# Kernel tuning notes

Hardware: AMD Instinct MI355X
Metric: run time of the kernel (lower is better)

## Reference

```python
import jax, jax.numpy as jnp
import numpy as np

B, H, S, D = 1, 16, 2048, 128
NUM_DOCS = 4


def setup_inputs() -> dict:
    key = jax.random.key(0)
    kq, kk, kv = jax.random.split(key, 3)
    q = jax.random.normal(kq, (B, H, S, D), dtype=jnp.float32)
    k = jax.random.normal(kk, (B, H, S, D), dtype=jnp.float32)
    v = jax.random.normal(kv, (B, H, S, D), dtype=jnp.float32)
    # Document boundaries within the packed sequence (as produced by _get_offsets):
    # starts at 0, ends at total token count. 4 equal docs of length 512.
    offsets = jnp.array([0, 512, 1024, 1536, 2048], dtype=jnp.int64)
    return {"q": q, "k": k, "v": v, "offsets": offsets}


def reference(q, k, v, offsets):
    # Block-causal SDPA: token i attends to token j iff j <= i and both are
    # in the same document (documents delimited by `offsets`). This matches
    # nested-tensor SDPA with is_causal=True over the jagged documents.
    _, _, S_, D_ = q.shape
    pos = jnp.arange(S_)
    seg = jnp.searchsorted(offsets, pos, side="right")  # [S] document id per token
    mask = (seg[:, None] == seg[None, :]) & (pos[None, :] <= pos[:, None])  # [S,S]
    scale = 1.0 / jnp.sqrt(jnp.asarray(D_, q.dtype))
    scores = jnp.einsum("bhsd,bhtd->bhst", q, k) * scale  # [B,H,S,S]
    scores = jnp.where(mask[None, None], scores, jnp.finfo(q.dtype).min)
    attn = jax.nn.softmax(scores, axis=-1)
    return jnp.einsum("bhst,bhtd->bhsd", attn, v)
```

## Files before the change

### kernel.cpp

```cpp
#include <hip/hip_runtime.h>
#include <hip/hip_bf16.h>
#include <math.h>

#define NH 16
#define SL 2048
#define DM 128

typedef float f32x4 __attribute__((ext_vector_type(4)));
typedef short s16x8 __attribute__((ext_vector_type(8)));
typedef short s16x4 __attribute__((ext_vector_type(4)));
typedef int   i32x4 __attribute__((ext_vector_type(4)));

static __device__ __forceinline__ unsigned short f2bfu(float f) {
  __hip_bfloat16 h = __float2bfloat16(f);
  return (unsigned short)__builtin_bit_cast(short, h);
}
static __device__ __forceinline__ short f2bf(float f) {
  __hip_bfloat16 h = __float2bfloat16(f);
  return __builtin_bit_cast(short, h);
}
static __device__ __forceinline__ unsigned pack2(float lo, float hi) {
  return (unsigned)f2bfu(lo) | ((unsigned)f2bfu(hi) << 16);
}

__global__ __launch_bounds__(512) void attn_bq128(
    const float* __restrict__ qg,
    const float* __restrict__ kg,
    const float* __restrict__ vg,
    const int* __restrict__ offs, int n_off,
    float* __restrict__ out)
{
  __shared__ __align__(16) char Kb[2][16384];
  __shared__ __align__(16) char Vb[2][16384];

  const int t    = threadIdx.x;
  const int lane = t & 63;
  const int w    = t >> 6;
  const int col  = lane & 15;
  const int g    = lane >> 4;

  const int b  = blockIdx.x;
  const int h  = b & 15;
  const int qb = 15 - (b >> 4);
  const int q0 = qb * 128;

  const float* qh = qg + (size_t)h * SL * DM;
  const float* kh = kg + (size_t)h * SL * DM;
  const float* vh = vg + (size_t)h * SL * DM;

  const float scale2 = 0.08838834764831843f * 1.4426950408889634f;

  const int qrow = q0 + 16 * w + col;

  int ov[8];
  #pragma unroll
  for (int ii = 0; ii < 8; ++ii) ov[ii] = (ii < n_off) ? offs[ii] : 0x7fffffff;
  int qstart = 0, kv_lo = 0;
  #pragma unroll
  for (int ii = 0; ii < 8; ++ii) {
    if (ov[ii] <= qrow) qstart = max(qstart, ov[ii]);
    if (ov[ii] <= q0)   kv_lo  = max(kv_lo, ov[ii]);
  }
  const int n = ((q0 + 128) - kv_lo) >> 6;

  s16x8 qf[4];
  #pragma unroll
  for (int kk = 0; kk < 4; ++kk) {
    const float* qp = qh + (size_t)qrow * DM + 32 * kk + 8 * g;
    f32x4 lo = *(const f32x4*)qp;
    f32x4 hi = *(const f32x4*)(qp + 4);
    s16x8 f;
    f[0] = f2bf(lo[0] * scale2); f[1] = f2bf(lo[1] * scale2);
    f[2] = f2bf(lo[2] * scale2); f[3] = f2bf(lo[3] * scale2);
    f[4] = f2bf(hi[0] * scale2); f[5] = f2bf(hi[1] * scale2);
    f[6] = f2bf(hi[2] * scale2); f[7] = f2bf(hi[3] * scale2);
    qf[kk] = f;
  }

  f32x4 acc[8];
  #pragma unroll
  for (int dt = 0; dt < 8; ++dt) { f32x4 zv = {0.f, 0.f, 0.f, 0.f}; acc[dt] = zv; }
  float m_ = -1e30f, l_ = 0.f;

  const int d0  = (t & 31) * 4;
  const int r0  = t >> 5;
  const int k0  = r0 * 4;
  const int rot = (t >> 1) & 3;
  f32x4 kr[4], vr[4];

#define LOADT(T) do {                                                         \
    const float* _ks = kh + (size_t)(kv_lo + ((T) << 6)) * DM;                \
    const float* _vs = vh + (size_t)(kv_lo + ((T) << 6)) * DM;                \
    _Pragma("unroll")                                                         \
    for (int _i = 0; _i < 4; ++_i)                                            \
      kr[_i] = *(const f32x4*)(_ks + (size_t)(r0 + 16 * _i) * DM + d0);       \
    _Pragma("unroll")                                                         \
    for (int _j = 0; _j < 4; ++_j)                                            \
      vr[_j] = *(const f32x4*)(_vs + (size_t)(k0 + _j) * DM + d0);            \
  } while (0)

#define WRITEKV(B) do {                                                       \
    _Pragma("unroll")                                                         \
    for (int _i = 0; _i < 4; ++_i) {                                          \
      int _r = r0 + 16 * _i;                                                  \
      s16x4 _b;                                                               \
      _b[0] = f2bf(kr[_i][0]); _b[1] = f2bf(kr[_i][1]);                       \
      _b[2] = f2bf(kr[_i][2]); _b[3] = f2bf(kr[_i][3]);                       \
      *(s16x4*)(&Kb[B][0] + ((_r * 256 + d0 * 2) ^ ((_r & 7) << 4))) = _b;    \
    }                                                                         \
    _Pragma("unroll")                                                         \
    for (int _di = 0; _di < 4; ++_di) {                                       \
      int _dd = (_di + rot) & 3;                                              \
      int _d  = d0 + _dd;                                                     \
      s16x4 _b;                                                               \
      _b[0] = f2bf(vr[0][_dd]); _b[1] = f2bf(vr[1][_dd]);                     \
      _b[2] = f2bf(vr[2][_dd]); _b[3] = f2bf(vr[3][_dd]);                     \
      *(s16x4*)(&Vb[B][0] + ((_d * 128 + k0 * 2) ^ ((_d & 7) << 4))) = _b;    \
    }                                                                         \
  } while (0)

  LOADT(0);
  WRITEKV(0);
  int cur = 0;

  const int srcA = col + 32 * (g & 1);
  const int srcB = srcA + 16;
  const bool hi2 = (g >> 1) != 0;

  for (int it = 0; it < n; ++it) {
    const int kv0 = kv_lo + (it << 6);
    __syncthreads();

    const bool pre = (it + 1 < n);
    if (pre) LOADT(it + 1);
    __builtin_amdgcn_sched_barrier(0);

    f32x4 st[4];
    #pragma unroll
    for (int kt = 0; kt < 4; ++kt) { f32x4 zv = {0.f, 0.f, 0.f, 0.f}; st[kt] = zv; }
    __builtin_amdgcn_s_setprio(1);
    #pragma unroll
    for (int kt = 0; kt < 4; ++kt) {
      int row = kt * 16 + col;
      #pragma unroll
      for (int kk = 0; kk < 4; ++kk) {
        s16x8 kf = *(const s16x8*)(&Kb[cur][0] + ((row * 256 + 64 * kk + 16 * g) ^ ((row & 7) << 4)));
        st[kt] = __builtin_amdgcn_mfma_f32_16x16x32_bf16(kf, qf[kk], st[kt], 0, 0, 0);
      }
    }
    __builtin_amdgcn_s_setprio(0);

    const bool needmask = __any((kv0 + 63 > qrow) || (kv0 < qstart));
    if (needmask) {
      #pragma unroll
      for (int kt = 0; kt < 4; ++kt) {
        #pragma unroll
        for (int r = 0; r < 4; ++r) {
          int kpos = kv0 + kt * 16 + 4 * g + r;
          bool ok = (kpos <= qrow) && (kpos >= qstart);
          st[kt][r] = ok ? st[kt][r] : -3.0e38f;
        }
      }
    }
    float cm = -3.0e38f;
    #pragma unroll
    for (int kt = 0; kt < 4; ++kt) {
      #pragma unroll
      for (int r = 0; r < 4; ++r) cm = fmaxf(cm, st[kt][r]);
    }
    cm = fmaxf(cm, __shfl_xor(cm, 16));
    cm = fmaxf(cm, __shfl_xor(cm, 32));
    float al = 1.f;
    float mn = m_;
    if (!__all(cm <= m_)) {
      mn = fmaxf(m_, cm);
      al = __builtin_amdgcn_exp2f(m_ - mn);
      m_ = mn;
      #pragma unroll
      for (int r = 0; r < 4; ++r) {
        float ar = __shfl(al, 4 * g + r);
        #pragma unroll
        for (int dt = 0; dt < 8; ++dt) acc[dt][r] *= ar;
      }
    }
    float psum = 0.f;
    unsigned w01[4], w23[4];
    #pragma unroll
    for (int kt = 0; kt < 4; ++kt) {
      float p0 = __builtin_amdgcn_exp2f(st[kt][0] - mn);
      float p1 = __builtin_amdgcn_exp2f(st[kt][1] - mn);
      float p2 = __builtin_amdgcn_exp2f(st[kt][2] - mn);
      float p3 = __builtin_amdgcn_exp2f(st[kt][3] - mn);
      psum += (p0 + p1) + (p2 + p3);
      w01[kt] = pack2(p0, p1);
      w23[kt] = pack2(p2, p3);
    }
    psum += __shfl_xor(psum, 16);
    psum += __shfl_xor(psum, 32);
    l_ = l_ * al + psum;

    __builtin_amdgcn_s_setprio(1);
    #pragma unroll
    for (int ksel = 0; ksel < 2; ++ksel) {
      unsigned a0 = __shfl(w01[2 * ksel], srcA);
      unsigned a1 = __shfl(w01[2 * ksel + 1], srcA);
      unsigned b0 = __shfl(w23[2 * ksel], srcA);
      unsigned b1 = __shfl(w23[2 * ksel + 1], srcA);
      unsigned c0 = __shfl(w01[2 * ksel], srcB);
      unsigned c1 = __shfl(w01[2 * ksel + 1], srcB);
      unsigned e0 = __shfl(w23[2 * ksel], srcB);
      unsigned e1 = __shfl(w23[2 * ksel + 1], srcB);
      i32x4 uu;
      uu[0] = (int)(hi2 ? a1 : a0);
      uu[1] = (int)(hi2 ? b1 : b0);
      uu[2] = (int)(hi2 ? c1 : c0);
      uu[3] = (int)(hi2 ? e1 : e0);
      s16x8 pa = __builtin_bit_cast(s16x8, uu);
      #pragma unroll
      for (int dt = 0; dt < 8; ++dt) {
        int d = dt * 16 + col;
        s16x8 vf = *(const s16x8*)(&Vb[cur][0] + ((d * 128 + 64 * ksel + 16 * g) ^ ((d & 7) << 4)));
        acc[dt] = __builtin_amdgcn_mfma_f32_16x16x32_bf16(pa, vf, acc[dt], 0, 0, 0);
      }
    }
    __builtin_amdgcn_s_setprio(0);

    if (pre) WRITEKV(cur ^ 1);
    cur ^= 1;
  }
#undef LOADT
#undef WRITEKV

  #pragma unroll
  for (int r = 0; r < 4; ++r) {
    float lr  = __shfl(l_, 4 * g + r);
    float inv = 1.f / lr;
    int row   = q0 + 16 * w + 4 * g + r;
    float* op = out + ((size_t)h * SL + row) * DM + col;
    #pragma unroll
    for (int dt = 0; dt < 8; ++dt) op[dt * 16] = acc[dt][r] * inv;
  }
}

extern "C" void kernel_launch(void* const* d_in, const int* in_sizes, int n_in,
                              void* d_out, int out_size, void* d_ws, size_t ws_size,
                              hipStream_t stream) {
  const float* q = (const float*)d_in[0];
  const float* k = (const float*)d_in[1];
  const float* v = (const float*)d_in[2];
  const int* offs = (const int*)d_in[3];
  const int n_off = in_sizes[3];
  float* out = (float*)d_out;

  const int blocks = NH * (SL / 128);
  attn_bq128<<<blocks, 512, 0, stream>>>(q, k, v, offs, n_off, out);
}
```

Before: 30.01 us.

## Widen KV tile to 128 rows and defer softmax cross-lane reductions

Doubles the K/V tile per iteration from 64 to 128 keys, doubling the LDS buffers and per-thread staging registers. This halves the number of loop iterations and barriers. The row max is now reduced across lanes only when some lane exceeds the running max. The row-sum shuffles are moved out of the loop to a single reduction at the end. The mask test becomes a uniform check (different doc start or last tile), in exchange for 128KB LDS per block and more VGPR pressure.

```diff
diff --git a/kernel.cpp b/kernel.cpp
--- a/kernel.cpp
+++ b/kernel.cpp
@@ -23,15 +23,15 @@
   return (unsigned)f2bfu(lo) | ((unsigned)f2bfu(hi) << 16);
 }
 
-__global__ __launch_bounds__(512) void attn_bq128(
+__global__ __launch_bounds__(512) void attn_k128(
     const float* __restrict__ qg,
     const float* __restrict__ kg,
     const float* __restrict__ vg,
     const int* __restrict__ offs, int n_off,
     float* __restrict__ out)
 {
-  __shared__ __align__(16) char Kb[2][16384];
-  __shared__ __align__(16) char Vb[2][16384];
+  __shared__ __align__(16) char Kb[2][32768];
+  __shared__ __align__(16) char Vb[2][32768];
 
   const int t    = threadIdx.x;
   const int lane = t & 63;
@@ -61,7 +61,9 @@
     if (ov[ii] <= qrow) qstart = max(qstart, ov[ii]);
     if (ov[ii] <= q0)   kv_lo  = max(kv_lo, ov[ii]);
   }
-  const int n = ((q0 + 128) - kv_lo) >> 6;
+  const int n = ((q0 + 128) - kv_lo) >> 7;
+
+  const bool qsdiff = __any(qstart != kv_lo);
 
   s16x8 qf[4];
   #pragma unroll
@@ -80,28 +82,29 @@
   f32x4 acc[8];
   #pragma unroll
   for (int dt = 0; dt < 8; ++dt) { f32x4 zv = {0.f, 0.f, 0.f, 0.f}; acc[dt] = zv; }
-  float m_ = -1e30f, l_ = 0.f;
+  float m_ = -1e30f;
+  float l_ = 0.f;
 
   const int d0  = (t & 31) * 4;
   const int r0  = t >> 5;
-  const int k0  = r0 * 4;
+  const int k0v = r0 * 8;
   const int rot = (t >> 1) & 3;
-  f32x4 kr[4], vr[4];
+  f32x4 kr[8], vr[8];
 
 #define LOADT(T) do {                                                         \
-    const float* _ks = kh + (size_t)(kv_lo + ((T) << 6)) * DM;                \
-    const float* _vs = vh + (size_t)(kv_lo + ((T) << 6)) * DM;                \
-    _Pragma("unroll")                                                         \
-    for (int _i = 0; _i < 4; ++_i)                                            \
+    const float* _ks = kh + (size_t)(kv_lo + ((T) << 7)) * DM;                \
+    const float* _vs = vh + (size_t)(kv_lo + ((T) << 7)) * DM;                \
+    _Pragma("unroll")                                                         \
+    for (int _i = 0; _i < 8; ++_i)                                            \
       kr[_i] = *(const f32x4*)(_ks + (size_t)(r0 + 16 * _i) * DM + d0);       \
     _Pragma("unroll")                                                         \
-    for (int _j = 0; _j < 4; ++_j)                                            \
-      vr[_j] = *(const f32x4*)(_vs + (size_t)(k0 + _j) * DM + d0);            \
+    for (int _j = 0; _j < 8; ++_j)                                            \
+      vr[_j] = *(const f32x4*)(_vs + (size_t)(k0v + _j) * DM + d0);           \
   } while (0)
 
 #define WRITEKV(B) do {                                                       \
     _Pragma("unroll")                                                         \
-    for (int _i = 0; _i < 4; ++_i) {                                          \
+    for (int _i = 0; _i < 8; ++_i) {                                          \
       int _r = r0 + 16 * _i;                                                  \
       s16x4 _b;                                                               \
       _b[0] = f2bf(kr[_i][0]); _b[1] = f2bf(kr[_i][1]);                       \
@@ -112,10 +115,12 @@
     for (int _di = 0; _di < 4; ++_di) {                                       \
       int _dd = (_di + rot) & 3;                                              \
       int _d  = d0 + _dd;                                                     \
-      s16x4 _b;                                                               \
-      _b[0] = f2bf(vr[0][_dd]); _b[1] = f2bf(vr[1][_dd]);                     \
-      _b[2] = f2bf(vr[2][_dd]); _b[3] = f2bf(vr[3][_dd]);                     \
-      *(s16x4*)(&Vb[B][0] + ((_d * 128 + k0 * 2) ^ ((_d & 7) << 4))) = _b;    \
+      s16x8 _b8;                                                              \
+      _b8[0] = f2bf(vr[0][_dd]); _b8[1] = f2bf(vr[1][_dd]);                   \
+      _b8[2] = f2bf(vr[2][_dd]); _b8[3] = f2bf(vr[3][_dd]);                   \
+      _b8[4] = f2bf(vr[4][_dd]); _b8[5] = f2bf(vr[5][_dd]);                   \
+      _b8[6] = f2bf(vr[6][_dd]); _b8[7] = f2bf(vr[7][_dd]);                   \
+      *(s16x8*)(&Vb[B][0] + ((_d * 256 + k0v * 2) ^ ((_d & 7) << 4))) = _b8;  \
     }                                                                         \
   } while (0)
 
@@ -128,19 +133,19 @@
   const bool hi2 = (g >> 1) != 0;
 
   for (int it = 0; it < n; ++it) {
-    const int kv0 = kv_lo + (it << 6);
+    const int kv0 = kv_lo + (it << 7);
     __syncthreads();
 
     const bool pre = (it + 1 < n);
     if (pre) LOADT(it + 1);
     __builtin_amdgcn_sched_barrier(0);
 
-    f32x4 st[4];
-    #pragma unroll
-    for (int kt = 0; kt < 4; ++kt) { f32x4 zv = {0.f, 0.f, 0.f, 0.f}; st[kt] = zv; }
+    f32x4 st[8];
+    #pragma unroll
+    for (int kt = 0; kt < 8; ++kt) { f32x4 zv = {0.f, 0.f, 0.f, 0.f}; st[kt] = zv; }
     __builtin_amdgcn_s_setprio(1);
     #pragma unroll
-    for (int kt = 0; kt < 4; ++kt) {
+    for (int kt = 0; kt < 8; ++kt) {
       int row = kt * 16 + col;
       #pragma unroll
       for (int kk = 0; kk < 4; ++kk) {
@@ -150,10 +155,10 @@
     }
     __builtin_amdgcn_s_setprio(0);
 
-    const bool needmask = __any((kv0 + 63 > qrow) || (kv0 < qstart));
+    const bool needmask = qsdiff || (it + 1 == n);
     if (needmask) {
       #pragma unroll
-      for (int kt = 0; kt < 4; ++kt) {
+      for (int kt = 0; kt < 8; ++kt) {
         #pragma unroll
         for (int r = 0; r < 4; ++r) {
           int kpos = kv0 + kt * 16 + 4 * g + r;
@@ -162,17 +167,19 @@
         }
       }
     }
-    float cm = -3.0e38f;
-    #pragma unroll
-    for (int kt = 0; kt < 4; ++kt) {
-      #pragma unroll
-      for (int r = 0; r < 4; ++r) cm = fmaxf(cm, st[kt][r]);
-    }
-    cm = fmaxf(cm, __shfl_xor(cm, 16));
-    cm = fmaxf(cm, __shfl_xor(cm, 32));
+
+    float mk[8];
+    #pragma unroll
+    for (int kt = 0; kt < 8; ++kt)
+      mk[kt] = fmaxf(fmaxf(st[kt][0], st[kt][1]), fmaxf(st[kt][2], st[kt][3]));
+    float cm = fmaxf(fmaxf(fmaxf(mk[0], mk[1]), fmaxf(mk[2], mk[3])),
+                     fmaxf(fmaxf(mk[4], mk[5]), fmaxf(mk[6], mk[7])));
+
     float al = 1.f;
     float mn = m_;
     if (!__all(cm <= m_)) {
+      cm = fmaxf(cm, __shfl_xor(cm, 16));
+      cm = fmaxf(cm, __shfl_xor(cm, 32));
       mn = fmaxf(m_, cm);
       al = __builtin_amdgcn_exp2f(m_ - mn);
       m_ = mn;
@@ -183,25 +190,25 @@
         for (int dt = 0; dt < 8; ++dt) acc[dt][r] *= ar;
       }
     }
-    float psum = 0.f;
-    unsigned w01[4], w23[4];
-    #pragma unroll
-    for (int kt = 0; kt < 4; ++kt) {
+
+    float ps[8];
+    unsigned w01[8], w23[8];
+    #pragma unroll
+    for (int kt = 0; kt < 8; ++kt) {
       float p0 = __builtin_amdgcn_exp2f(st[kt][0] - mn);
       float p1 = __builtin_amdgcn_exp2f(st[kt][1] - mn);
       float p2 = __builtin_amdgcn_exp2f(st[kt][2] - mn);
       float p3 = __builtin_amdgcn_exp2f(st[kt][3] - mn);
-      psum += (p0 + p1) + (p2 + p3);
+      ps[kt] = (p0 + p1) + (p2 + p3);
       w01[kt] = pack2(p0, p1);
       w23[kt] = pack2(p2, p3);
     }
-    psum += __shfl_xor(psum, 16);
-    psum += __shfl_xor(psum, 32);
-    l_ = l_ * al + psum;
+    l_ = l_ * al + (((ps[0] + ps[1]) + (ps[2] + ps[3])) +
+                    ((ps[4] + ps[5]) + (ps[6] + ps[7])));
 
     __builtin_amdgcn_s_setprio(1);
     #pragma unroll
-    for (int ksel = 0; ksel < 2; ++ksel) {
+    for (int ksel = 0; ksel < 4; ++ksel) {
       unsigned a0 = __shfl(w01[2 * ksel], srcA);
       unsigned a1 = __shfl(w01[2 * ksel + 1], srcA);
       unsigned b0 = __shfl(w23[2 * ksel], srcA);
@@ -219,7 +226,7 @@
       #pragma unroll
       for (int dt = 0; dt < 8; ++dt) {
         int d = dt * 16 + col;
-        s16x8 vf = *(const s16x8*)(&Vb[cur][0] + ((d * 128 + 64 * ksel + 16 * g) ^ ((d & 7) << 4)));
+        s16x8 vf = *(const s16x8*)(&Vb[cur][0] + ((d * 256 + 64 * ksel + 16 * g) ^ ((d & 7) << 4)));
         acc[dt] = __builtin_amdgcn_mfma_f32_16x16x32_bf16(pa, vf, acc[dt], 0, 0, 0);
       }
     }
@@ -231,9 +238,12 @@
 #undef LOADT
 #undef WRITEKV
 
+  float l0 = l_;
+  l0 += __shfl_xor(l0, 16);
+  l0 += __shfl_xor(l0, 32);
   #pragma unroll
   for (int r = 0; r < 4; ++r) {
-    float lr  = __shfl(l_, 4 * g + r);
+    float lr  = __shfl(l0, 4 * g + r);
     float inv = 1.f / lr;
     int row   = q0 + 16 * w + 4 * g + r;
     float* op = out + ((size_t)h * SL + row) * DM + col;
@@ -253,5 +263,5 @@
   float* out = (float*)d_out;
 
   const int blocks = NH * (SL / 128);
-  attn_bq128<<<blocks, 512, 0, stream>>>(q, k, v, offs, n_off, out);
-}
+  attn_k128<<<blocks, 512, 0, stream>>>(q, k, v, offs, n_off, out);
+}
```

New measurement: 29.13 us. 1.03x faster.
